# Kernel tuning notes

Hardware: AMD Instinct MI355X
Metric: run time of the kernel (lower is better)

## Reference

```python
import jax, jax.numpy as jnp
import numpy as np

N_NODES = 50000
N_EDGES = 800000
NODE_DIM = 256
EDGE_DIM = 64
HIDDEN = 512
OUT_DIM = 256


def setup_inputs() -> dict:
    key = jax.random.key(0)
    ks = jax.random.split(key, 6)
    node_features = jax.random.normal(ks[0], (N_NODES, NODE_DIM), dtype=jnp.float32)
    edge_index = jax.random.randint(ks[1], (2, N_EDGES), 0, N_NODES, dtype=jnp.int64)
    edge_features = jax.random.normal(ks[2], (N_EDGES, EDGE_DIM), dtype=jnp.float32)
    in_dim = EDGE_DIM + NODE_DIM
    W1 = jax.random.normal(ks[3], (in_dim, HIDDEN), dtype=jnp.float32) * (1.0 / np.sqrt(in_dim))
    b1 = jnp.zeros((HIDDEN,), dtype=jnp.float32)
    W2 = jax.random.normal(ks[4], (HIDDEN, OUT_DIM), dtype=jnp.float32) * (1.0 / np.sqrt(HIDDEN))
    b2 = jnp.zeros((OUT_DIM,), dtype=jnp.float32)
    return {"node_features": node_features, "edge_index": edge_index,
            "edge_features": edge_features, "W1": W1, "b1": b1, "W2": W2, "b2": b2}


def reference(node_features, edge_index, edge_features, W1, b1, W2, b2):
    # edge_direction='in' -> scatter edge features to target nodes (row 1)
    tgt = edge_index[1]
    # mean aggregation: segment-sum of features and counts, clamp counts at 1
    agg = jax.ops.segment_sum(edge_features, tgt, num_segments=N_NODES)  # [N, E_dim]
    counts = jax.ops.segment_sum(jnp.ones((edge_features.shape[0],), edge_features.dtype),
                                 tgt, num_segments=N_NODES)
    agg = agg / jnp.maximum(counts, 1.0)[:, None]
    combined = jnp.concatenate([agg, node_features], axis=1)  # [N, edge+node]
    h = jax.nn.relu(combined @ W1 + b1)  # dropout=0 -> identity
    out = h @ W2 + b2  # [N, OUT_DIM]
    return out
```

## Files before the change

kernel.cpp:

```cpp
#include <hip/hip_runtime.h>
#include <hip/hip_bf16.h>

#define N_NODES 50000
#define N_EDGES 800000
#define NODE_DIM 256
#define EDGE_DIM 64
#define HIDDEN 512
#define OUT_DIM 256
#define IN_DIM 320
#define SCAN_BLOCKS ((N_NODES + 255) / 256)
#define HIST_BLOCKS ((N_EDGES + 255) / 256)
#define CW_ELEMS (IN_DIM * HIDDEN + HIDDEN * OUT_DIM)
#define CW_BLOCKS ((CW_ELEMS + 255) / 256)

typedef __bf16 bf16_t;
typedef bf16_t bf16x8 __attribute__((ext_vector_type(8)));
typedef bf16_t bf16x4 __attribute__((ext_vector_type(4)));
typedef float floatx4 __attribute__((ext_vector_type(4)));

__device__ inline bf16_t to_bf16(float f) {
    __hip_bfloat16 h = __float2bfloat16(f);
    bf16_t b;
    __builtin_memcpy(&b, &h, 2);
    return b;
}

__device__ inline void async16(const void* g, void* l) {
    __builtin_amdgcn_global_load_lds(
        (const __attribute__((address_space(1))) unsigned int*)g,
        (__attribute__((address_space(3))) unsigned int*)l, 16, 0, 0);
}

__global__ __launch_bounds__(256) void hist_and_weights(
    const int* __restrict__ eidx, int* __restrict__ counts,
    const float* __restrict__ W1, const float* __restrict__ W2,
    bf16_t* __restrict__ W1T, bf16_t* __restrict__ W2T) {
    if (blockIdx.x < HIST_BLOCKS) {
        int e = blockIdx.x * 256 + threadIdx.x;
        if (e >= N_EDGES) return;
        int t = min(max(eidx[N_EDGES + e], 0), N_NODES - 1);
        atomicAdd(&counts[t], 1);
    } else {
        int idx = (blockIdx.x - HIST_BLOCKS) * 256 + threadIdx.x;
        if (idx < IN_DIM * HIDDEN) {
            int k = idx / HIDDEN, n = idx - k * HIDDEN;
            W1T[(size_t)n * IN_DIM + k] = to_bf16(W1[idx]);
        } else {
            int j = idx - IN_DIM * HIDDEN;
            if (j < HIDDEN * OUT_DIM) {
                int k = j / OUT_DIM, n = j - k * OUT_DIM;
                W2T[(size_t)n * HIDDEN + k] = to_bf16(W2[j]);
            }
        }
    }
}

__global__ __launch_bounds__(256) void scan_blocks(
    const int* __restrict__ counts, int* __restrict__ local_excl,
    int* __restrict__ blocksums) {
    __shared__ int s[256];
    int t = threadIdx.x;
    int idx = blockIdx.x * 256 + t;
    int v = (idx < N_NODES) ? counts[idx] : 0;
    s[t] = v;
    __syncthreads();
#pragma unroll
    for (int off = 1; off < 256; off <<= 1) {
        int u = (t >= off) ? s[t - off] : 0;
        __syncthreads();
        s[t] += u;
        __syncthreads();
    }
    if (idx < N_NODES) local_excl[idx] = s[t] - v;
    if (t == 255) blocksums[blockIdx.x] = s[255];
}

__global__ __launch_bounds__(256) void scan_sums(
    const int* __restrict__ blocksums, int* __restrict__ scanned,
    int* __restrict__ offsets) {
    __shared__ int s[256];
    int t = threadIdx.x;
    int v = (t < SCAN_BLOCKS) ? blocksums[t] : 0;
    s[t] = v;
    __syncthreads();
#pragma unroll
    for (int off = 1; off < 256; off <<= 1) {
        int u = (t >= off) ? s[t - off] : 0;
        __syncthreads();
        s[t] += u;
        __syncthreads();
    }
    if (t < SCAN_BLOCKS) scanned[t] = s[t] - v;
    if (t == 255) offsets[N_NODES] = s[255];
}

__global__ __launch_bounds__(256) void add_base(
    const int* __restrict__ local_excl, const int* __restrict__ scanned,
    int* __restrict__ offsets, int* __restrict__ cursor) {
    int idx = blockIdx.x * 256 + threadIdx.x;
    if (idx >= N_NODES) return;
    int o = local_excl[idx] + scanned[blockIdx.x];
    offsets[idx] = o;
    cursor[idx] = o;
}

__global__ __launch_bounds__(256) void scatter_ids(
    const int* __restrict__ eidx, int* __restrict__ cursor,
    int* __restrict__ sorted) {
    int e = blockIdx.x * 256 + threadIdx.x;
    if (e >= N_EDGES) return;
    int t = min(max(eidx[N_EDGES + e], 0), N_NODES - 1);
    int pos = atomicAdd(&cursor[t], 1);
    sorted[pos] = e;
}

__global__ __launch_bounds__(256) void gather_combined(
    const float* __restrict__ ef, const int* __restrict__ sorted,
    const int* __restrict__ offsets, const float* __restrict__ node,
    bf16_t* __restrict__ combined) {
    int wave = (blockIdx.x * 256 + threadIdx.x) >> 6;
    int lane = threadIdx.x & 63;
    if (wave >= N_NODES) return;
    const int slot = lane >> 4;
    const int g4 = lane & 15;

    int beg = offsets[wave], end = offsets[wave + 1];
    int deg = end - beg;

    int myidx = (lane < deg) ? sorted[beg + lane] : -1;

    floatx4 acc = {0.f, 0.f, 0.f, 0.f};
    int nfull = min(deg, 64);
    for (int j = 0; j < nfull; j += 4) {
        int eid = __shfl(myidx, j + slot);
        if (j + slot < nfull) {
            floatx4 v = *reinterpret_cast<const floatx4*>(
                &ef[(size_t)eid * EDGE_DIM + g4 * 4]);
            acc += v;
        }
    }
    for (int j = 64; j < deg; j += 4) {
        int js = j + slot;
        if (js < deg) {
            int eid = sorted[beg + js];
            floatx4 v = *reinterpret_cast<const floatx4*>(
                &ef[(size_t)eid * EDGE_DIM + g4 * 4]);
            acc += v;
        }
    }

#pragma unroll
    for (int m = 16; m <= 32; m <<= 1) {
        acc[0] += __shfl_xor(acc[0], m);
        acc[1] += __shfl_xor(acc[1], m);
        acc[2] += __shfl_xor(acc[2], m);
        acc[3] += __shfl_xor(acc[3], m);
    }

    float inv = 1.0f / (float)max(deg, 1);
    size_t cb = (size_t)wave * IN_DIM;
    if (slot == 0) {
        bf16x4 o;
        o[0] = to_bf16(acc[0] * inv);
        o[1] = to_bf16(acc[1] * inv);
        o[2] = to_bf16(acc[2] * inv);
        o[3] = to_bf16(acc[3] * inv);
        *reinterpret_cast<bf16x4*>(&combined[cb + g4 * 4]) = o;
    }
    floatx4 nv = *reinterpret_cast<const floatx4*>(
        &node[(size_t)wave * NODE_DIM + lane * 4]);
    bf16x4 no;
    no[0] = to_bf16(nv[0]);
    no[1] = to_bf16(nv[1]);
    no[2] = to_bf16(nv[2]);
    no[3] = to_bf16(nv[3]);
    *reinterpret_cast<bf16x4*>(&combined[cb + EDGE_DIM + lane * 4]) = no;
}

template <bool RELU, bool OUT_BF16>
__global__ __launch_bounds__(256) void gemm_bt(
    const bf16_t* __restrict__ A, const bf16_t* __restrict__ BT,
    const float* __restrict__ bias, void* __restrict__ Cout,
    int M, int N, int K) {
    __shared__ bf16_t As[128][32];
    __shared__ bf16_t Bs[128][32];

    const int tid = threadIdx.x;
    const int lane = tid & 63;
    const int w = tid >> 6;
    const int wm = (w & 1) * 64;
    const int wn = (w >> 1) * 64;
    const int lrow = lane & 15;
    const int quad = lane >> 4;
    const int kq = quad * 8;
    const int m0 = blockIdx.x * 128;
    const int n0 = blockIdx.y * 128;

    floatx4 acc[4][4] = {};

    const int nkt = K / 32;
    for (int kt = 0; kt < nkt; ++kt) {
        const int k0 = kt * 32;
        __syncthreads();
#pragma unroll
        for (int it = 0; it < 2; ++it) {
            int slot = it * 256 + tid;
            int row = slot >> 2;
            int cg = (slot & 3) * 8;
            int gm = min(m0 + row, M - 1);
            async16(&A[(size_t)gm * K + k0 + cg], (bf16_t*)As + slot * 8);
            async16(&BT[(size_t)(n0 + row) * K + k0 + cg], (bf16_t*)Bs + slot * 8);
        }
        __syncthreads();

        bf16x8 af[4], bfr[4];
#pragma unroll
        for (int mi = 0; mi < 4; ++mi)
            af[mi] = *reinterpret_cast<const bf16x8*>(&As[wm + mi * 16 + lrow][kq]);
#pragma unroll
        for (int ni = 0; ni < 4; ++ni)
            bfr[ni] = *reinterpret_cast<const bf16x8*>(&Bs[wn + ni * 16 + lrow][kq]);
#pragma unroll
        for (int mi = 0; mi < 4; ++mi)
#pragma unroll
            for (int ni = 0; ni < 4; ++ni)
                acc[mi][ni] = __builtin_amdgcn_mfma_f32_16x16x32_bf16(
                    af[mi], bfr[ni], acc[mi][ni], 0, 0, 0);
    }

#pragma unroll
    for (int ni = 0; ni < 4; ++ni) {
        int gn = n0 + wn + ni * 16 + lrow;
        float bv = bias[gn];
#pragma unroll
        for (int mi = 0; mi < 4; ++mi) {
            int gmb = m0 + wm + mi * 16 + quad * 4;
#pragma unroll
            for (int r = 0; r < 4; ++r) {
                int gm = gmb + r;
                if (gm < M) {
                    float v = acc[mi][ni][r] + bv;
                    if (RELU) v = fmaxf(v, 0.0f);
                    if (OUT_BF16)
                        ((bf16_t*)Cout)[(size_t)gm * N + gn] = to_bf16(v);
                    else
                        ((float*)Cout)[(size_t)gm * N + gn] = v;
                }
            }
        }
    }
}

extern "C" void kernel_launch(void* const* d_in, const int* in_sizes, int n_in,
                              void* d_out, int out_size, void* d_ws, size_t ws_size,
                              hipStream_t stream) {
    const float* node = (const float*)d_in[0];
    const int* eidx = (const int*)d_in[1];
    const float* ef = (const float*)d_in[2];
    const float* W1 = (const float*)d_in[3];
    const float* b1 = (const float*)d_in[4];
    const float* W2 = (const float*)d_in[5];
    const float* b2 = (const float*)d_in[6];
    float* out = (float*)d_out;

    char* ws = (char*)d_ws;
    int* counts = (int*)ws;
    int* offsets = (int*)(ws + 200000);
    int* cursor = (int*)(ws + 400016);
    int* sorted = (int*)(ws + 600016);
    int* local_excl = (int*)(ws + 3800016);
    int* blocksums = (int*)(ws + 4000016);
    int* scanned = (int*)(ws + 4000800);
    bf16_t* combined = (bf16_t*)(ws + 4001600);
    bf16_t* h = (bf16_t*)(ws + 36001600);
    bf16_t* W1T = (bf16_t*)(ws + 87201600);
    bf16_t* W2T = (bf16_t*)(ws + 87529280);

    hipMemsetAsync(counts, 0, 200000, stream);

    hist_and_weights<<<HIST_BLOCKS + CW_BLOCKS, 256, 0, stream>>>(
        eidx, counts, W1, W2, W1T, W2T);
    scan_blocks<<<SCAN_BLOCKS, 256, 0, stream>>>(counts, local_excl, blocksums);
    scan_sums<<<1, 256, 0, stream>>>(blocksums, scanned, offsets);
    add_base<<<SCAN_BLOCKS, 256, 0, stream>>>(local_excl, scanned, offsets, cursor);
    scatter_ids<<<(N_EDGES + 255) / 256, 256, 0, stream>>>(eidx, cursor, sorted);
    gather_combined<<<(N_NODES * 64 + 255) / 256, 256, 0, stream>>>(
        ef, sorted, offsets, node, combined);

    gemm_bt<true, true><<<dim3((N_NODES + 127) / 128, HIDDEN / 128), 256, 0, stream>>>(
        combined, W1T, b1, (void*)h, N_NODES, HIDDEN, IN_DIM);

    gemm_bt<false, false><<<dim3((N_NODES + 127) / 128, OUT_DIM / 128), 256, 0, stream>>>(
        h, W2T, b2, (void*)out, N_NODES, OUT_DIM, HIDDEN);
}
```

Before: 559.7 us.

## Replace CSR sort-and-gather with float atomic scatter aggregation

Drops the counting-sort pipeline (histogram, three scan kernels, scatter of edge ids, per-node gather) and instead accumulates edge features straight into a float aggregate buffer with atomicAdd, then normalises by count while building the bf16 combined matrix. This cuts the number of kernel launches and the serial scan stages, but issues 51.2M float atomics to L2. It also makes the sum order nondeterministic. The workspace layout is reorganised so h aliases the agg buffer.

```diff
diff --git a/kernel.cpp b/kernel.cpp
--- a/kernel.cpp
+++ b/kernel.cpp
@@ -8,10 +8,11 @@
 #define HIDDEN 512
 #define OUT_DIM 256
 #define IN_DIM 320
-#define SCAN_BLOCKS ((N_NODES + 255) / 256)
-#define HIST_BLOCKS ((N_EDGES + 255) / 256)
+
+#define SCAT_BLOCKS ((N_EDGES * 16) / 256)
 #define CW_ELEMS (IN_DIM * HIDDEN + HIDDEN * OUT_DIM)
 #define CW_BLOCKS ((CW_ELEMS + 255) / 256)
+#define BC_THREADS (N_NODES * 80)
 
 typedef __bf16 bf16_t;
 typedef bf16_t bf16x8 __attribute__((ext_vector_type(8)));
@@ -31,17 +32,28 @@
         (__attribute__((address_space(3))) unsigned int*)l, 16, 0, 0);
 }
 
-__global__ __launch_bounds__(256) void hist_and_weights(
-    const int* __restrict__ eidx, int* __restrict__ counts,
+__global__ __launch_bounds__(256) void scatter_and_weights(
+    const int* __restrict__ eidx, const float* __restrict__ ef,
+    float* __restrict__ agg, int* __restrict__ counts,
     const float* __restrict__ W1, const float* __restrict__ W2,
     bf16_t* __restrict__ W1T, bf16_t* __restrict__ W2T) {
-    if (blockIdx.x < HIST_BLOCKS) {
-        int e = blockIdx.x * 256 + threadIdx.x;
-        if (e >= N_EDGES) return;
-        int t = min(max(eidx[N_EDGES + e], 0), N_NODES - 1);
-        atomicAdd(&counts[t], 1);
+    if (blockIdx.x < SCAT_BLOCKS) {
+        int gid = blockIdx.x * 256 + threadIdx.x;
+        int e = gid >> 4;
+        int q = gid & 15;
+        if (e < N_EDGES) {
+            int t = min(max(eidx[N_EDGES + e], 0), N_NODES - 1);
+            floatx4 v = *reinterpret_cast<const floatx4*>(
+                &ef[(size_t)e * EDGE_DIM + q * 4]);
+            float* dst = &agg[(size_t)t * EDGE_DIM + q * 4];
+            atomicAdd(dst + 0, v[0]);
+            atomicAdd(dst + 1, v[1]);
+            atomicAdd(dst + 2, v[2]);
+            atomicAdd(dst + 3, v[3]);
+            if (q == 0) atomicAdd(&counts[t], 1);
+        }
     } else {
-        int idx = (blockIdx.x - HIST_BLOCKS) * 256 + threadIdx.x;
+        int idx = (blockIdx.x - SCAT_BLOCKS) * 256 + threadIdx.x;
         if (idx < IN_DIM * HIDDEN) {
             int k = idx / HIDDEN, n = idx - k * HIDDEN;
             W1T[(size_t)n * IN_DIM + k] = to_bf16(W1[idx]);
@@ -55,126 +67,28 @@
     }
 }
 
-__global__ __launch_bounds__(256) void scan_blocks(
-    const int* __restrict__ counts, int* __restrict__ local_excl,
-    int* __restrict__ blocksums) {
-    __shared__ int s[256];
-    int t = threadIdx.x;
-    int idx = blockIdx.x * 256 + t;
-    int v = (idx < N_NODES) ? counts[idx] : 0;
-    s[t] = v;
-    __syncthreads();
-#pragma unroll
-    for (int off = 1; off < 256; off <<= 1) {
-        int u = (t >= off) ? s[t - off] : 0;
-        __syncthreads();
-        s[t] += u;
-        __syncthreads();
-    }
-    if (idx < N_NODES) local_excl[idx] = s[t] - v;
-    if (t == 255) blocksums[blockIdx.x] = s[255];
-}
-
-__global__ __launch_bounds__(256) void scan_sums(
-    const int* __restrict__ blocksums, int* __restrict__ scanned,
-    int* __restrict__ offsets) {
-    __shared__ int s[256];
-    int t = threadIdx.x;
-    int v = (t < SCAN_BLOCKS) ? blocksums[t] : 0;
-    s[t] = v;
-    __syncthreads();
-#pragma unroll
-    for (int off = 1; off < 256; off <<= 1) {
-        int u = (t >= off) ? s[t - off] : 0;
-        __syncthreads();
-        s[t] += u;
-        __syncthreads();
-    }
-    if (t < SCAN_BLOCKS) scanned[t] = s[t] - v;
-    if (t == 255) offsets[N_NODES] = s[255];
-}
-
-__global__ __launch_bounds__(256) void add_base(
-    const int* __restrict__ local_excl, const int* __restrict__ scanned,
-    int* __restrict__ offsets, int* __restrict__ cursor) {
+__global__ __launch_bounds__(256) void build_combined(
+    const float* __restrict__ agg, const int* __restrict__ counts,
+    const float* __restrict__ node, bf16_t* __restrict__ combined) {
     int idx = blockIdx.x * 256 + threadIdx.x;
-    if (idx >= N_NODES) return;
-    int o = local_excl[idx] + scanned[blockIdx.x];
-    offsets[idx] = o;
-    cursor[idx] = o;
-}
-
-__global__ __launch_bounds__(256) void scatter_ids(
-    const int* __restrict__ eidx, int* __restrict__ cursor,
-    int* __restrict__ sorted) {
-    int e = blockIdx.x * 256 + threadIdx.x;
-    if (e >= N_EDGES) return;
-    int t = min(max(eidx[N_EDGES + e], 0), N_NODES - 1);
-    int pos = atomicAdd(&cursor[t], 1);
-    sorted[pos] = e;
-}
-
-__global__ __launch_bounds__(256) void gather_combined(
-    const float* __restrict__ ef, const int* __restrict__ sorted,
-    const int* __restrict__ offsets, const float* __restrict__ node,
-    bf16_t* __restrict__ combined) {
-    int wave = (blockIdx.x * 256 + threadIdx.x) >> 6;
-    int lane = threadIdx.x & 63;
-    if (wave >= N_NODES) return;
-    const int slot = lane >> 4;
-    const int g4 = lane & 15;
-
-    int beg = offsets[wave], end = offsets[wave + 1];
-    int deg = end - beg;
-
-    int myidx = (lane < deg) ? sorted[beg + lane] : -1;
-
-    floatx4 acc = {0.f, 0.f, 0.f, 0.f};
-    int nfull = min(deg, 64);
-    for (int j = 0; j < nfull; j += 4) {
-        int eid = __shfl(myidx, j + slot);
-        if (j + slot < nfull) {
-            floatx4 v = *reinterpret_cast<const floatx4*>(
-                &ef[(size_t)eid * EDGE_DIM + g4 * 4]);
-            acc += v;
-        }
-    }
-    for (int j = 64; j < deg; j += 4) {
-        int js = j + slot;
-        if (js < deg) {
-            int eid = sorted[beg + js];
-            floatx4 v = *reinterpret_cast<const floatx4*>(
-                &ef[(size_t)eid * EDGE_DIM + g4 * 4]);
-            acc += v;
-        }
-    }
-
-#pragma unroll
-    for (int m = 16; m <= 32; m <<= 1) {
-        acc[0] += __shfl_xor(acc[0], m);
-        acc[1] += __shfl_xor(acc[1], m);
-        acc[2] += __shfl_xor(acc[2], m);
-        acc[3] += __shfl_xor(acc[3], m);
-    }
-
-    float inv = 1.0f / (float)max(deg, 1);
-    size_t cb = (size_t)wave * IN_DIM;
-    if (slot == 0) {
-        bf16x4 o;
-        o[0] = to_bf16(acc[0] * inv);
-        o[1] = to_bf16(acc[1] * inv);
-        o[2] = to_bf16(acc[2] * inv);
-        o[3] = to_bf16(acc[3] * inv);
-        *reinterpret_cast<bf16x4*>(&combined[cb + g4 * 4]) = o;
-    }
-    floatx4 nv = *reinterpret_cast<const floatx4*>(
-        &node[(size_t)wave * NODE_DIM + lane * 4]);
-    bf16x4 no;
-    no[0] = to_bf16(nv[0]);
-    no[1] = to_bf16(nv[1]);
-    no[2] = to_bf16(nv[2]);
-    no[3] = to_bf16(nv[3]);
-    *reinterpret_cast<bf16x4*>(&combined[cb + EDGE_DIM + lane * 4]) = no;
+    if (idx >= BC_THREADS) return;
+    int n = idx / 80;
+    int q = idx - n * 80;
+    floatx4 v;
+    if (q < 16) {
+        v = *reinterpret_cast<const floatx4*>(&agg[(size_t)n * EDGE_DIM + q * 4]);
+        float inv = 1.0f / (float)max(counts[n], 1);
+        v *= inv;
+    } else {
+        v = *reinterpret_cast<const floatx4*>(
+            &node[(size_t)n * NODE_DIM + (q - 16) * 4]);
+    }
+    bf16x4 o;
+    o[0] = to_bf16(v[0]);
+    o[1] = to_bf16(v[1]);
+    o[2] = to_bf16(v[2]);
+    o[3] = to_bf16(v[3]);
+    *reinterpret_cast<bf16x4*>(&combined[(size_t)n * IN_DIM + q * 4]) = o;
 }
 
 template <bool RELU, bool OUT_BF16>
@@ -264,28 +178,20 @@
     float* out = (float*)d_out;
 
     char* ws = (char*)d_ws;
-    int* counts = (int*)ws;
-    int* offsets = (int*)(ws + 200000);
-    int* cursor = (int*)(ws + 400016);
-    int* sorted = (int*)(ws + 600016);
-    int* local_excl = (int*)(ws + 3800016);
-    int* blocksums = (int*)(ws + 4000016);
-    int* scanned = (int*)(ws + 4000800);
-    bf16_t* combined = (bf16_t*)(ws + 4001600);
-    bf16_t* h = (bf16_t*)(ws + 36001600);
-    bf16_t* W1T = (bf16_t*)(ws + 87201600);
-    bf16_t* W2T = (bf16_t*)(ws + 87529280);
-
-    hipMemsetAsync(counts, 0, 200000, stream);
-
-    hist_and_weights<<<HIST_BLOCKS + CW_BLOCKS, 256, 0, stream>>>(
-        eidx, counts, W1, W2, W1T, W2T);
-    scan_blocks<<<SCAN_BLOCKS, 256, 0, stream>>>(counts, local_excl, blocksums);
-    scan_sums<<<1, 256, 0, stream>>>(blocksums, scanned, offsets);
-    add_base<<<SCAN_BLOCKS, 256, 0, stream>>>(local_excl, scanned, offsets, cursor);
-    scatter_ids<<<(N_EDGES + 255) / 256, 256, 0, stream>>>(eidx, cursor, sorted);
-    gather_combined<<<(N_NODES * 64 + 255) / 256, 256, 0, stream>>>(
-        ef, sorted, offsets, node, combined);
+    float* agg = (float*)ws;
+    int* counts = (int*)(ws + 12800000);
+    bf16_t* h = (bf16_t*)ws;
+    bf16_t* combined = (bf16_t*)(ws + 51200000);
+    bf16_t* W1T = (bf16_t*)(ws + 83200000);
+    bf16_t* W2T = (bf16_t*)(ws + 83527680);
+
+    hipMemsetAsync(ws, 0, 13000000, stream);
+
+    scatter_and_weights<<<SCAT_BLOCKS + CW_BLOCKS, 256, 0, stream>>>(
+        eidx, ef, agg, counts, W1, W2, W1T, W2T);
+
+    build_combined<<<BC_THREADS / 256, 256, 0, stream>>>(
+        agg, counts, node, combined);
 
     gemm_bt<true, true><<<dim3((N_NODES + 127) / 128, HIDDEN / 128), 256, 0, stream>>>(
         combined, W1T, b1, (void*)h, N_NODES, HIDDEN, IN_DIM);
```

Result: slower. 1.086 ms (+94.1%).

## Fuse CSR build and gather into one persistent kernel with grid barriers

Applied to the files above, without the earlier changes.

Replaces the memset plus six front-end kernels (histogram, weight conversion, two-level scan, base add, scatter, gather) with a single persistent kernel of 512 blocks. Phases are separated by software grid barriers built on global atomics, and each scan chunk recomputes its base by summing all earlier counts instead of using a separate block-sum kernel. The aim is to remove launch gaps and tail effects between the many small kernels. In exchange it relies on all 512 blocks being co-resident, which could deadlock otherwise, and the redundant prefix summation adds extra reads.

```diff
diff --git a/kernel.cpp b/kernel.cpp
--- a/kernel.cpp
+++ b/kernel.cpp
@@ -8,10 +8,11 @@
 #define HIDDEN 512
 #define OUT_DIM 256
 #define IN_DIM 320
-#define SCAN_BLOCKS ((N_NODES + 255) / 256)
-#define HIST_BLOCKS ((N_EDGES + 255) / 256)
-#define CW_ELEMS (IN_DIM * HIDDEN + HIDDEN * OUT_DIM)
-#define CW_BLOCKS ((CW_ELEMS + 255) / 256)
+
+#define FRONT_BLOCKS 512
+#define FT (FRONT_BLOCKS * 256)
+#define TOTAL_WAVES (FT / 64)
+#define SCAN_CHUNKS 196
 
 typedef __bf16 bf16_t;
 typedef bf16_t bf16x8 __attribute__((ext_vector_type(8)));
@@ -31,150 +32,170 @@
         (__attribute__((address_space(3))) unsigned int*)l, 16, 0, 0);
 }
 
-__global__ __launch_bounds__(256) void hist_and_weights(
-    const int* __restrict__ eidx, int* __restrict__ counts,
-    const float* __restrict__ W1, const float* __restrict__ W2,
-    bf16_t* __restrict__ W1T, bf16_t* __restrict__ W2T) {
-    if (blockIdx.x < HIST_BLOCKS) {
-        int e = blockIdx.x * 256 + threadIdx.x;
-        if (e >= N_EDGES) return;
-        int t = min(max(eidx[N_EDGES + e], 0), N_NODES - 1);
-        atomicAdd(&counts[t], 1);
-    } else {
-        int idx = (blockIdx.x - HIST_BLOCKS) * 256 + threadIdx.x;
-        if (idx < IN_DIM * HIDDEN) {
-            int k = idx / HIDDEN, n = idx - k * HIDDEN;
-            W1T[(size_t)n * IN_DIM + k] = to_bf16(W1[idx]);
+__device__ int g_bar_count[8];
+__device__ int g_bar_release[8];
+
+__device__ inline void gbar(int k) {
+    __syncthreads();
+    if (threadIdx.x == 0) {
+        int gen = __hip_atomic_load(&g_bar_release[k], __ATOMIC_RELAXED,
+                                    __HIP_MEMORY_SCOPE_AGENT);
+        __threadfence();
+        int old = atomicAdd(&g_bar_count[k], 1);
+        if (old == FRONT_BLOCKS - 1) {
+            atomicExch(&g_bar_count[k], 0);
+            __threadfence();
+            atomicAdd(&g_bar_release[k], 1);
         } else {
-            int j = idx - IN_DIM * HIDDEN;
-            if (j < HIDDEN * OUT_DIM) {
-                int k = j / OUT_DIM, n = j - k * OUT_DIM;
-                W2T[(size_t)n * HIDDEN + k] = to_bf16(W2[j]);
-            }
-        }
-    }
-}
-
-__global__ __launch_bounds__(256) void scan_blocks(
-    const int* __restrict__ counts, int* __restrict__ local_excl,
-    int* __restrict__ blocksums) {
+            while (__hip_atomic_load(&g_bar_release[k], __ATOMIC_RELAXED,
+                                     __HIP_MEMORY_SCOPE_AGENT) == gen)
+                __builtin_amdgcn_s_sleep(2);
+        }
+        __threadfence();
+    }
+    __syncthreads();
+}
+
+__global__ __launch_bounds__(256, 2) void fused_front(
+    const float* __restrict__ node, const int* __restrict__ eidx,
+    const float* __restrict__ ef, const float* __restrict__ W1,
+    const float* __restrict__ W2, char* __restrict__ ws) {
     __shared__ int s[256];
-    int t = threadIdx.x;
-    int idx = blockIdx.x * 256 + t;
-    int v = (idx < N_NODES) ? counts[idx] : 0;
-    s[t] = v;
-    __syncthreads();
-#pragma unroll
-    for (int off = 1; off < 256; off <<= 1) {
-        int u = (t >= off) ? s[t - off] : 0;
-        __syncthreads();
-        s[t] += u;
-        __syncthreads();
-    }
-    if (idx < N_NODES) local_excl[idx] = s[t] - v;
-    if (t == 255) blocksums[blockIdx.x] = s[255];
-}
-
-__global__ __launch_bounds__(256) void scan_sums(
-    const int* __restrict__ blocksums, int* __restrict__ scanned,
-    int* __restrict__ offsets) {
-    __shared__ int s[256];
-    int t = threadIdx.x;
-    int v = (t < SCAN_BLOCKS) ? blocksums[t] : 0;
-    s[t] = v;
-    __syncthreads();
-#pragma unroll
-    for (int off = 1; off < 256; off <<= 1) {
-        int u = (t >= off) ? s[t - off] : 0;
-        __syncthreads();
-        s[t] += u;
-        __syncthreads();
-    }
-    if (t < SCAN_BLOCKS) scanned[t] = s[t] - v;
-    if (t == 255) offsets[N_NODES] = s[255];
-}
-
-__global__ __launch_bounds__(256) void add_base(
-    const int* __restrict__ local_excl, const int* __restrict__ scanned,
-    int* __restrict__ offsets, int* __restrict__ cursor) {
-    int idx = blockIdx.x * 256 + threadIdx.x;
-    if (idx >= N_NODES) return;
-    int o = local_excl[idx] + scanned[blockIdx.x];
-    offsets[idx] = o;
-    cursor[idx] = o;
-}
-
-__global__ __launch_bounds__(256) void scatter_ids(
-    const int* __restrict__ eidx, int* __restrict__ cursor,
-    int* __restrict__ sorted) {
-    int e = blockIdx.x * 256 + threadIdx.x;
-    if (e >= N_EDGES) return;
-    int t = min(max(eidx[N_EDGES + e], 0), N_NODES - 1);
-    int pos = atomicAdd(&cursor[t], 1);
-    sorted[pos] = e;
-}
-
-__global__ __launch_bounds__(256) void gather_combined(
-    const float* __restrict__ ef, const int* __restrict__ sorted,
-    const int* __restrict__ offsets, const float* __restrict__ node,
-    bf16_t* __restrict__ combined) {
-    int wave = (blockIdx.x * 256 + threadIdx.x) >> 6;
-    int lane = threadIdx.x & 63;
-    if (wave >= N_NODES) return;
-    const int slot = lane >> 4;
-    const int g4 = lane & 15;
-
-    int beg = offsets[wave], end = offsets[wave + 1];
-    int deg = end - beg;
-
-    int myidx = (lane < deg) ? sorted[beg + lane] : -1;
-
-    floatx4 acc = {0.f, 0.f, 0.f, 0.f};
-    int nfull = min(deg, 64);
-    for (int j = 0; j < nfull; j += 4) {
-        int eid = __shfl(myidx, j + slot);
-        if (j + slot < nfull) {
-            floatx4 v = *reinterpret_cast<const floatx4*>(
-                &ef[(size_t)eid * EDGE_DIM + g4 * 4]);
-            acc += v;
-        }
-    }
-    for (int j = 64; j < deg; j += 4) {
-        int js = j + slot;
-        if (js < deg) {
-            int eid = sorted[beg + js];
-            floatx4 v = *reinterpret_cast<const floatx4*>(
-                &ef[(size_t)eid * EDGE_DIM + g4 * 4]);
-            acc += v;
-        }
-    }
-
-#pragma unroll
-    for (int m = 16; m <= 32; m <<= 1) {
-        acc[0] += __shfl_xor(acc[0], m);
-        acc[1] += __shfl_xor(acc[1], m);
-        acc[2] += __shfl_xor(acc[2], m);
-        acc[3] += __shfl_xor(acc[3], m);
-    }
-
-    float inv = 1.0f / (float)max(deg, 1);
-    size_t cb = (size_t)wave * IN_DIM;
-    if (slot == 0) {
-        bf16x4 o;
-        o[0] = to_bf16(acc[0] * inv);
-        o[1] = to_bf16(acc[1] * inv);
-        o[2] = to_bf16(acc[2] * inv);
-        o[3] = to_bf16(acc[3] * inv);
-        *reinterpret_cast<bf16x4*>(&combined[cb + g4 * 4]) = o;
-    }
-    floatx4 nv = *reinterpret_cast<const floatx4*>(
-        &node[(size_t)wave * NODE_DIM + lane * 4]);
-    bf16x4 no;
-    no[0] = to_bf16(nv[0]);
-    no[1] = to_bf16(nv[1]);
-    no[2] = to_bf16(nv[2]);
-    no[3] = to_bf16(nv[3]);
-    *reinterpret_cast<bf16x4*>(&combined[cb + EDGE_DIM + lane * 4]) = no;
+
+    int* counts = (int*)ws;
+    int* offsets = (int*)(ws + 200000);
+    int* cursor = (int*)(ws + 400016);
+    int* sorted = (int*)(ws + 600016);
+    bf16_t* combined = (bf16_t*)(ws + 4001600);
+    bf16_t* W1T = (bf16_t*)(ws + 87201600);
+    bf16_t* W2T = (bf16_t*)(ws + 87529280);
+
+    const int tid = threadIdx.x;
+    const int b = blockIdx.x;
+    const int gtid = b * 256 + tid;
+
+    for (int i = gtid; i < N_NODES; i += FT) counts[i] = 0;
+    for (int idx = gtid; idx < IN_DIM * HIDDEN; idx += FT) {
+        int k = idx / HIDDEN, n = idx - k * HIDDEN;
+        W1T[(size_t)n * IN_DIM + k] = to_bf16(W1[idx]);
+    }
+    for (int idx = gtid; idx < HIDDEN * OUT_DIM; idx += FT) {
+        int k = idx / OUT_DIM, n = idx - k * OUT_DIM;
+        W2T[(size_t)n * HIDDEN + k] = to_bf16(W2[idx]);
+    }
+    gbar(0);
+
+    for (int e = gtid; e < N_EDGES; e += FT) {
+        int tg = min(max(eidx[N_EDGES + e], 0), N_NODES - 1);
+        atomicAdd(&counts[tg], 1);
+    }
+    gbar(1);
+
+    if (b < SCAN_CHUNKS) {
+        const int chunk0 = b * 256;
+        int part = 0;
+        for (int i = tid; i < chunk0; i += 256)
+            part += __hip_atomic_load(&counts[i], __ATOMIC_RELAXED,
+                                      __HIP_MEMORY_SCOPE_AGENT);
+        s[tid] = part;
+        __syncthreads();
+#pragma unroll
+        for (int off = 128; off > 0; off >>= 1) {
+            if (tid < off) s[tid] += s[tid + off];
+            __syncthreads();
+        }
+        int base = s[0];
+        __syncthreads();
+
+        int idx = chunk0 + tid;
+        int v = (idx < N_NODES)
+                    ? __hip_atomic_load(&counts[idx], __ATOMIC_RELAXED,
+                                        __HIP_MEMORY_SCOPE_AGENT)
+                    : 0;
+        s[tid] = v;
+        __syncthreads();
+#pragma unroll
+        for (int off = 1; off < 256; off <<= 1) {
+            int u = (tid >= off) ? s[tid - off] : 0;
+            __syncthreads();
+            s[tid] += u;
+            __syncthreads();
+        }
+        if (idx < N_NODES) {
+            int o = base + s[tid] - v;
+            offsets[idx] = o;
+            cursor[idx] = o;
+        }
+        if (b == 0 && tid == 0) offsets[N_NODES] = N_EDGES;
+    }
+    gbar(2);
+
+    for (int e = gtid; e < N_EDGES; e += FT) {
+        int tg = min(max(eidx[N_EDGES + e], 0), N_NODES - 1);
+        int pos = atomicAdd(&cursor[tg], 1);
+        sorted[pos] = e;
+    }
+    gbar(3);
+
+    {
+        const int wv0 = gtid >> 6;
+        const int lane = tid & 63;
+        const int slot = lane >> 4;
+        const int g4 = lane & 15;
+        for (int n = wv0; n < N_NODES; n += TOTAL_WAVES) {
+            int beg = offsets[n], end = offsets[n + 1];
+            int deg = end - beg;
+
+            int myidx = (lane < deg) ? sorted[beg + lane] : -1;
+
+            floatx4 acc = {0.f, 0.f, 0.f, 0.f};
+            int nfull = min(deg, 64);
+            for (int j = 0; j < nfull; j += 4) {
+                int eid = __shfl(myidx, j + slot);
+                if (j + slot < nfull) {
+                    floatx4 v = *reinterpret_cast<const floatx4*>(
+                        &ef[(size_t)eid * EDGE_DIM + g4 * 4]);
+                    acc += v;
+                }
+            }
+            for (int j = 64; j < deg; j += 4) {
+                int js = j + slot;
+                if (js < deg) {
+                    int eid = sorted[beg + js];
+                    floatx4 v = *reinterpret_cast<const floatx4*>(
+                        &ef[(size_t)eid * EDGE_DIM + g4 * 4]);
+                    acc += v;
+                }
+            }
+
+#pragma unroll
+            for (int m = 16; m <= 32; m <<= 1) {
+                acc[0] += __shfl_xor(acc[0], m);
+                acc[1] += __shfl_xor(acc[1], m);
+                acc[2] += __shfl_xor(acc[2], m);
+                acc[3] += __shfl_xor(acc[3], m);
+            }
+
+            float inv = 1.0f / (float)max(deg, 1);
+            size_t cb = (size_t)n * IN_DIM;
+            if (slot == 0) {
+                bf16x4 o;
+                o[0] = to_bf16(acc[0] * inv);
+                o[1] = to_bf16(acc[1] * inv);
+                o[2] = to_bf16(acc[2] * inv);
+                o[3] = to_bf16(acc[3] * inv);
+                *reinterpret_cast<bf16x4*>(&combined[cb + g4 * 4]) = o;
+            }
+            floatx4 nv = *reinterpret_cast<const floatx4*>(
+                &node[(size_t)n * NODE_DIM + lane * 4]);
+            bf16x4 no;
+            no[0] = to_bf16(nv[0]);
+            no[1] = to_bf16(nv[1]);
+            no[2] = to_bf16(nv[2]);
+            no[3] = to_bf16(nv[3]);
+            *reinterpret_cast<bf16x4*>(&combined[cb + EDGE_DIM + lane * 4]) = no;
+        }
+    }
 }
 
 template <bool RELU, bool OUT_BF16>
@@ -264,28 +285,12 @@
     float* out = (float*)d_out;
 
     char* ws = (char*)d_ws;
-    int* counts = (int*)ws;
-    int* offsets = (int*)(ws + 200000);
-    int* cursor = (int*)(ws + 400016);
-    int* sorted = (int*)(ws + 600016);
-    int* local_excl = (int*)(ws + 3800016);
-    int* blocksums = (int*)(ws + 4000016);
-    int* scanned = (int*)(ws + 4000800);
     bf16_t* combined = (bf16_t*)(ws + 4001600);
     bf16_t* h = (bf16_t*)(ws + 36001600);
     bf16_t* W1T = (bf16_t*)(ws + 87201600);
     bf16_t* W2T = (bf16_t*)(ws + 87529280);
 
-    hipMemsetAsync(counts, 0, 200000, stream);
-
-    hist_and_weights<<<HIST_BLOCKS + CW_BLOCKS, 256, 0, stream>>>(
-        eidx, counts, W1, W2, W1T, W2T);
-    scan_blocks<<<SCAN_BLOCKS, 256, 0, stream>>>(counts, local_excl, blocksums);
-    scan_sums<<<1, 256, 0, stream>>>(blocksums, scanned, offsets);
-    add_base<<<SCAN_BLOCKS, 256, 0, stream>>>(local_excl, scanned, offsets, cursor);
-    scatter_ids<<<(N_EDGES + 255) / 256, 256, 0, stream>>>(eidx, cursor, sorted);
-    gather_combined<<<(N_NODES * 64 + 255) / 256, 256, 0, stream>>>(
-        ef, sorted, offsets, node, combined);
+    fused_front<<<FRONT_BLOCKS, 256, 0, stream>>>(node, eidx, ef, W1, W2, ws);
 
     gemm_bt<true, true><<<dim3((N_NODES + 127) / 128, HIDDEN / 128), 256, 0, stream>>>(
         combined, W1T, b1, (void*)h, N_NODES, HIDDEN, IN_DIM);
```

Result: slower. 706.8 us (+26.3%).
